# Kernel optimization log

Hardware: AMD Instinct MI355X
Metric: run time of the kernel (lower is better)

The kernel has to match this reference:

```python
import jax, jax.numpy as jnp
import numpy as np

EPS = 1e-7  # keras backend.epsilon()
NUM_ROUTING = 3


def squash(v, axis=-1):
    s2 = jnp.sum(jnp.square(v), axis=axis, keepdims=True)
    scale = s2 / (1.0 + s2) / jnp.sqrt(s2 + EPS)
    return scale * v


def setup_inputs() -> dict:
    key = jax.random.key(0)
    k1, k2 = jax.random.split(key)
    B, I, Q = 64, 2048, 16      # batch, input_num_capsule, input_dim_capsule
    J, P = 32, 32               # num_capsule, dim_capsule
    inputs = jax.random.normal(k1, (B, I, Q), dtype=jnp.float32)
    # glorot-ish scale for W: [num_capsule, input_num_capsule, dim_capsule, input_dim_capsule]
    W = jax.random.normal(k2, (J, I, P, Q), dtype=jnp.float32) * (1.0 / np.sqrt(Q))
    return {"inputs": inputs, "W": W}


def reference(inputs, W):
    # inputs_hat[b,j,i,p] = sum_q inputs[b,i,q] * W[j,i,p,q]
    hat = jnp.einsum('biq,jipq->bjip', inputs, W)
    hat_stop = jax.lax.stop_gradient(hat)
    B, J, I, P = hat.shape
    b = jnp.zeros((B, J, I), dtype=hat.dtype)
    for _ in range(NUM_ROUTING - 1):
        c = jax.nn.softmax(b, axis=1)                       # softmax over num_capsule axis
        v = squash(jnp.einsum('bji,bjip->bjp', c, hat_stop))
        b = b + jnp.einsum('bjp,bjip->bji', v, hat_stop)
    c = jax.nn.softmax(b, axis=1)
    return squash(jnp.einsum('bji,bjip->bjp', c, hat))      # [B, J, P]
```

## Files before the change

### kernel.cpp

```cpp
#include <hip/hip_runtime.h>

typedef _Float16 h8 __attribute__((ext_vector_type(8)));
typedef _Float16 h4 __attribute__((ext_vector_type(4)));
typedef float f4 __attribute__((ext_vector_type(4)));

constexpr int NB = 64;
constexpr int NI = 2048;
constexpr int NQ = 16;
constexpr int NJ = 32;
constexpr int NP = 32;
constexpr int NIP = NI / 2;
constexpr int VSZ = NB * NJ * NP;


__global__ __launch_bounds__(256)
void zero_kernel(f4* __restrict__ p)
{
    const f4 z = {0.f, 0.f, 0.f, 0.f};
    p[(size_t)blockIdx.x * 256 + threadIdx.x] = z;
}

__global__ __launch_bounds__(256)
void xpack_kernel(const float* __restrict__ X, h8* __restrict__ xp)
{
    const int ip = blockIdx.x;
    const int t = threadIdx.x;
    const int bf = t >> 6, l = t & 63;
    const int b = (l & 15) + 16 * bf;
    const int i = 2 * ip + (l >= 32 ? 1 : 0);
    const int q0 = ((l >> 4) & 1) * 8;
    const float* xs = X + ((size_t)b * NI + i) * NQ + q0;
    const float4 u = *reinterpret_cast<const float4*>(xs);
    const float4 v = *reinterpret_cast<const float4*>(xs + 4);
    h8 h;
    h[0] = (_Float16)u.x; h[1] = (_Float16)u.y; h[2] = (_Float16)u.z; h[3] = (_Float16)u.w;
    h[4] = (_Float16)v.x; h[5] = (_Float16)v.y; h[6] = (_Float16)v.z; h[7] = (_Float16)v.w;
    xp[(size_t)(ip * 4 + bf) * 64 + l] = h;
}

__device__ inline float sqscale(float s2)
{
    return s2 / ((1.f + s2) * sqrtf(s2 + 1e-7f));
}

__global__ __launch_bounds__(512)
void wacc_kernel(const float* __restrict__ Wg, const h8* __restrict__ xp,
                 h8* __restrict__ wp, float* __restrict__ ACC)
{
    const int t = threadIdx.x, wv = t >> 6, l = t & 63;
    const int j = blockIdx.x >> 4, is = blockIdx.x & 15;
    const int ioff = (l >= 32) ? 1 : 0;
    const int q0 = ((l >> 4) & 1) * 8;
    const int pbase = is * 64 + wv * 8;

    f4 D[2][4];
#pragma unroll
    for (int pf = 0; pf < 2; ++pf)
#pragma unroll
        for (int bf = 0; bf < 4; ++bf) { f4 Z = {0.f, 0.f, 0.f, 0.f}; D[pf][bf] = Z; }

    const float* wgl = Wg + ((size_t)j * NI + ioff) * (NP * NQ) + (size_t)(l & 15) * NQ + q0;

    f4 u0, u1, v0, v1;
    {
        const float* s0 = wgl + (size_t)(2 * pbase) * (NP * NQ);
        u0 = *reinterpret_cast<const f4*>(s0);
        u1 = *reinterpret_cast<const f4*>(s0 + 4);
        v0 = *reinterpret_cast<const f4*>(s0 + 16 * NQ);
        v1 = *reinterpret_cast<const f4*>(s0 + 16 * NQ + 4);
    }
    h8 B0, B1, B2, B3;
    {
        const h8* xpb = xp + (size_t)pbase * 4 * 64 + l;
        B0 = xpb[0]; B1 = xpb[64]; B2 = xpb[128]; B3 = xpb[192];
    }

#pragma unroll 1
    for (int ipl = 0; ipl < 8; ++ipl) {
        const int ipg = pbase + ipl;
        const int nip = (ipl < 7) ? ipg + 1 : ipg;
        f4 nu0, nu1, nv0, nv1;
        {
            const float* s0 = wgl + (size_t)(2 * nip) * (NP * NQ);
            nu0 = *reinterpret_cast<const f4*>(s0);
            nu1 = *reinterpret_cast<const f4*>(s0 + 4);
            nv0 = *reinterpret_cast<const f4*>(s0 + 16 * NQ);
            nv1 = *reinterpret_cast<const f4*>(s0 + 16 * NQ + 4);
        }
        h8 nB0, nB1, nB2, nB3;
        {
            const h8* xpb = xp + (size_t)nip * 4 * 64 + l;
            nB0 = xpb[0]; nB1 = xpb[64]; nB2 = xpb[128]; nB3 = xpb[192];
        }

        h8 A0, A1;
#pragma unroll
        for (int e = 0; e < 4; ++e) {
            A0[e] = (_Float16)u0[e]; A0[e + 4] = (_Float16)u1[e];
            A1[e] = (_Float16)v0[e]; A1[e + 4] = (_Float16)v1[e];
        }
        const size_t wo = ((size_t)j * NIP + ipg) * 2 * 64 + l;
        wp[wo] = A0;
        wp[wo + 64] = A1;
        D[0][0] = __builtin_amdgcn_mfma_f32_16x16x32_f16(A0, B0, D[0][0], 0, 0, 0);
        D[1][0] = __builtin_amdgcn_mfma_f32_16x16x32_f16(A1, B0, D[1][0], 0, 0, 0);
        D[0][1] = __builtin_amdgcn_mfma_f32_16x16x32_f16(A0, B1, D[0][1], 0, 0, 0);
        D[1][1] = __builtin_amdgcn_mfma_f32_16x16x32_f16(A1, B1, D[1][1], 0, 0, 0);
        D[0][2] = __builtin_amdgcn_mfma_f32_16x16x32_f16(A0, B2, D[0][2], 0, 0, 0);
        D[1][2] = __builtin_amdgcn_mfma_f32_16x16x32_f16(A1, B2, D[1][2], 0, 0, 0);
        D[0][3] = __builtin_amdgcn_mfma_f32_16x16x32_f16(A0, B3, D[0][3], 0, 0, 0);
        D[1][3] = __builtin_amdgcn_mfma_f32_16x16x32_f16(A1, B3, D[1][3], 0, 0, 0);
        u0 = nu0; u1 = nu1; v0 = nv0; v1 = nv1;
        B0 = nB0; B1 = nB1; B2 = nB2; B3 = nB3;
    }

    __shared__ float R[8][64 * 36];
#pragma unroll
    for (int pf = 0; pf < 2; ++pf)
#pragma unroll
        for (int bf = 0; bf < 4; ++bf) {
            const int b = (l & 15) + 16 * bf, p = (l >> 4) * 4 + 16 * pf;
            *reinterpret_cast<f4*>(&R[wv][b * 36 + p]) = D[pf][bf];
        }
    __syncthreads();
#pragma unroll
    for (int k = 0; k < 4; ++k) {
        const int id = t + k * 512;
        const int b = id >> 5, p = id & 31;
        float s = 0.f;
#pragma unroll
        for (int w8 = 0; w8 < 8; ++w8) s += R[w8][b * 36 + p];
        atomicAdd(ACC + ((size_t)b * NJ + j) * NP + p, s);
    }
}

template <int SMODE>
__global__ __launch_bounds__(512)
void logits_kernel(const h8* __restrict__ wp, const h8* __restrict__ xp,
                   const float* __restrict__ U1, const float* __restrict__ U2,
                   _Float16* __restrict__ cp)
{
    __shared__ float L[8][32][64];
    const int t = threadIdx.x, wv = t >> 6, l = t & 63;
    const int i0 = blockIdx.x * 8;
    const int ip0 = blockIdx.x * 4;
    const bool lo = l >= 32;
    h8 zh;
#pragma unroll
    for (int e = 0; e < 8; ++e) zh[e] = (_Float16)0.f;

#pragma unroll 1
    for (int jj = 0; jj < 4; ++jj) {
        const int j = wv * 4 + jj;

        float sreg[4][8];
#pragma unroll
        for (int bf = 0; bf < 4; ++bf) {
            const int b = (l & 15) + 16 * bf;
            const size_t base = ((size_t)b * NJ + j) * NP + (l >> 4) * 4;
            float va[8];
#pragma unroll
            for (int pf = 0; pf < 2; ++pf) {
                const f4 u = *reinterpret_cast<const f4*>(U1 + base + 16 * pf);
#pragma unroll
                for (int r = 0; r < 4; ++r) va[pf * 4 + r] = u[r] * (1.f / 32.f);
            }
            float s2 = 0.f;
#pragma unroll
            for (int e = 0; e < 8; ++e) s2 += va[e] * va[e];
            s2 += __shfl_xor(s2, 16);
            s2 += __shfl_xor(s2, 32);
            const float sc1 = sqscale(s2);
#pragma unroll
            for (int e = 0; e < 8; ++e) sreg[bf][e] = va[e] * sc1;

            if (SMODE == 1) {
                float vb[8];
#pragma unroll
                for (int pf = 0; pf < 2; ++pf) {
                    const f4 u = *reinterpret_cast<const f4*>(U2 + base + 16 * pf);
#pragma unroll
                    for (int r = 0; r < 4; ++r) vb[pf * 4 + r] = u[r];
                }
                float t2 = 0.f;
#pragma unroll
                for (int e = 0; e < 8; ++e) t2 += vb[e] * vb[e];
                t2 += __shfl_xor(t2, 16);
                t2 += __shfl_xor(t2, 32);
                const float sc2 = sqscale(t2);
#pragma unroll
                for (int e = 0; e < 8; ++e) sreg[bf][e] += vb[e] * sc2;
            }
        }

        const h8* wj = wp + (size_t)j * NIP * 2 * 64 + l;
        h8 A0 = wj[(size_t)ip0 * 128];
        h8 A1 = wj[(size_t)ip0 * 128 + 64];

#pragma unroll 1
        for (int ipl = 0; ipl < 4; ++ipl) {
            const int ipg = ip0 + ipl;
            const int nip = (ipl < 3) ? ipg + 1 : ipg;
            h8 nA0 = wj[(size_t)nip * 128];
            h8 nA1 = wj[(size_t)nip * 128 + 64];

            const h8* xpb = xp + (size_t)ipg * 4 * 64 + l;
            h8 B[4];
#pragma unroll
            for (int bf = 0; bf < 4; ++bf) B[bf] = xpb[bf * 64];

#pragma unroll
            for (int half = 0; half < 2; ++half) {
                f4 D[2][4];
#pragma unroll
                for (int pf = 0; pf < 2; ++pf)
#pragma unroll
                    for (int bf = 0; bf < 4; ++bf) { f4 Z = {0.f, 0.f, 0.f, 0.f}; D[pf][bf] = Z; }
#pragma unroll
                for (int bf = 0; bf < 4; ++bf) {
                    const h8 Bm = ((half == 0) == lo) ? zh : B[bf];
                    D[0][bf] = __builtin_amdgcn_mfma_f32_16x16x32_f16(A0, Bm, D[0][bf], 0, 0, 0);
                    D[1][bf] = __builtin_amdgcn_mfma_f32_16x16x32_f16(A1, Bm, D[1][bf], 0, 0, 0);
                }
                float part[4];
#pragma unroll
                for (int bf = 0; bf < 4; ++bf) {
                    float p_ = 0.f;
#pragma unroll
                    for (int pf = 0; pf < 2; ++pf)
#pragma unroll
                        for (int r = 0; r < 4; ++r) p_ += sreg[bf][pf * 4 + r] * D[pf][bf][r];
                    p_ += __shfl_xor(p_, 16);
                    p_ += __shfl_xor(p_, 32);
                    part[bf] = p_;
                }
                const int hb = l >> 4;
                const float wval = hb == 0 ? part[0] : hb == 1 ? part[1] : hb == 2 ? part[2] : part[3];
                L[ipl * 2 + half][j][(l & 15) + 16 * hb] = wval;
            }
            A0 = nA0; A1 = nA1;
        }
    }
    __syncthreads();

    {
        const int b = t & 63, ii = t >> 6;
        float lv[32];
        float m = -1e30f;
#pragma unroll
        for (int j = 0; j < 32; ++j) { lv[j] = L[ii][j][b]; m = fmaxf(m, lv[j]); }
        float s = 0.f;
#pragma unroll
        for (int j = 0; j < 32; ++j) { lv[j] = __expf(lv[j] - m); s += lv[j]; }
        const float inv = 1.f / s;
#pragma unroll
        for (int j = 0; j < 32; ++j) L[ii][j][b] = lv[j] * inv;
    }
    __syncthreads();

    {
        const int jw = t >> 4, r = t & 15;
#pragma unroll 1
        for (int ii = 0; ii < 8; ++ii) {
            h4 c4;
#pragma unroll
            for (int e = 0; e < 4; ++e) c4[e] = (_Float16)L[ii][jw][16 * e + r];
            *reinterpret_cast<h4*>(cp + ((size_t)jw * NI + i0 + ii) * 64 + r * 4) = c4;
        }
    }
}

__global__ __launch_bounds__(512)
void accum_kernel(const h8* __restrict__ wp, const h8* __restrict__ xp,
                  const _Float16* __restrict__ cp, float* __restrict__ ACC)
{
    const int t = threadIdx.x, wv = t >> 6, l = t & 63;
    const int j = blockIdx.x >> 4, is = blockIdx.x & 15;
    const int ioff = (l >= 32) ? 1 : 0;

    f4 D[2][4];
#pragma unroll
    for (int pf = 0; pf < 2; ++pf)
#pragma unroll
        for (int bf = 0; bf < 4; ++bf) { f4 Z = {0.f, 0.f, 0.f, 0.f}; D[pf][bf] = Z; }

    const int pbase = is * 64 + wv * 8;
    const h8* wj = wp + (size_t)j * NIP * 2 * 64 + l;
    const _Float16* cj = cp + ((size_t)j * NI + ioff) * 64 + (l & 15) * 4;

    h8 A0 = wj[(size_t)pbase * 128];
    h8 A1 = wj[(size_t)pbase * 128 + 64];
    h8 B0, B1, B2, B3;
    {
        const h8* xpb = xp + (size_t)pbase * 4 * 64 + l;
        B0 = xpb[0]; B1 = xpb[64]; B2 = xpb[128]; B3 = xpb[192];
    }
    h4 c4 = *reinterpret_cast<const h4*>(cj + (size_t)(2 * pbase) * 64);

#pragma unroll 1
    for (int ipl = 0; ipl < 8; ++ipl) {
        const int ipg = pbase + ipl;
        const int nip = (ipl < 7) ? ipg + 1 : ipg;
        h8 nA0 = wj[(size_t)nip * 128];
        h8 nA1 = wj[(size_t)nip * 128 + 64];
        h8 nB0, nB1, nB2, nB3;
        {
            const h8* xpb = xp + (size_t)nip * 4 * 64 + l;
            nB0 = xpb[0]; nB1 = xpb[64]; nB2 = xpb[128]; nB3 = xpb[192];
        }
        h4 nc4 = *reinterpret_cast<const h4*>(cj + (size_t)(2 * nip) * 64);

        h8 b0 = B0 * c4[0], b1 = B1 * c4[1], b2 = B2 * c4[2], b3 = B3 * c4[3];
        D[0][0] = __builtin_amdgcn_mfma_f32_16x16x32_f16(A0, b0, D[0][0], 0, 0, 0);
        D[1][0] = __builtin_amdgcn_mfma_f32_16x16x32_f16(A1, b0, D[1][0], 0, 0, 0);
        D[0][1] = __builtin_amdgcn_mfma_f32_16x16x32_f16(A0, b1, D[0][1], 0, 0, 0);
        D[1][1] = __builtin_amdgcn_mfma_f32_16x16x32_f16(A1, b1, D[1][1], 0, 0, 0);
        D[0][2] = __builtin_amdgcn_mfma_f32_16x16x32_f16(A0, b2, D[0][2], 0, 0, 0);
        D[1][2] = __builtin_amdgcn_mfma_f32_16x16x32_f16(A1, b2, D[1][2], 0, 0, 0);
        D[0][3] = __builtin_amdgcn_mfma_f32_16x16x32_f16(A0, b3, D[0][3], 0, 0, 0);
        D[1][3] = __builtin_amdgcn_mfma_f32_16x16x32_f16(A1, b3, D[1][3], 0, 0, 0);
        A0 = nA0; A1 = nA1; B0 = nB0; B1 = nB1; B2 = nB2; B3 = nB3; c4 = nc4;
    }

    __shared__ float R[8][64 * 36];
#pragma unroll
    for (int pf = 0; pf < 2; ++pf)
#pragma unroll
        for (int bf = 0; bf < 4; ++bf) {
            const int b = (l & 15) + 16 * bf, p = (l >> 4) * 4 + 16 * pf;
            *reinterpret_cast<f4*>(&R[wv][b * 36 + p]) = D[pf][bf];
        }
    __syncthreads();
#pragma unroll
    for (int k = 0; k < 4; ++k) {
        const int id = t + k * 512;
        const int b = id >> 5, p = id & 31;
        float s = 0.f;
#pragma unroll
        for (int w8 = 0; w8 < 8; ++w8) s += R[w8][b * 36 + p];
        atomicAdd(ACC + ((size_t)b * NJ + j) * NP + p, s);
    }
}

__global__ __launch_bounds__(256)
void squash_kernel(const float* __restrict__ U, float* __restrict__ OUT)
{
    const int t   = threadIdx.x;
    const int row = blockIdx.x * 8 + (t >> 5);
    const int p   = t & 31;
    const float val = U[row * 32 + p];
    float sq = val * val;
#pragma unroll
    for (int d = 1; d < 32; d <<= 1) sq += __shfl_xor(sq, d);
    OUT[row * 32 + p] = val * sqscale(sq);
}

extern "C" void kernel_launch(void* const* d_in, const int* in_sizes, int n_in,
                              void* d_out, int out_size, void* d_ws, size_t ws_size,
                              hipStream_t stream)
{
    const float* X  = (const float*)d_in[0];
    const float* Wg = (const float*)d_in[1];
    float* out = (float*)d_out;

    float* v1u = (float*)d_ws;
    float* v2u = v1u + VSZ;
    float* ou  = v2u + VSZ;
    h8* xp = (h8*)((char*)d_ws + (size_t)3 * VSZ * 4);
    _Float16* cp = (_Float16*)((char*)xp + (size_t)NIP * 4 * 64 * 16);
    h8* wpk = (h8*)((char*)cp + (size_t)NJ * NI * 64 * 2);

    xpack_kernel<<<NIP, 256, 0, stream>>>(X, xp);
    zero_kernel<<<3 * VSZ * 4 / (256 * 16), 256, 0, stream>>>((f4*)d_ws);

    wacc_kernel<<<512, 512, 0, stream>>>(Wg, xp, wpk, v1u);

    logits_kernel<0><<<NI / 8, 512, 0, stream>>>(wpk, xp, v1u, nullptr, cp);
    accum_kernel<<<512, 512, 0, stream>>>(wpk, xp, cp, v2u);

    logits_kernel<1><<<NI / 8, 512, 0, stream>>>(wpk, xp, v1u, v2u, cp);
    accum_kernel<<<512, 512, 0, stream>>>(wpk, xp, cp, ou);

    squash_kernel<<<VSZ / 256, 256, 0, stream>>>(ou, out);
}
```

Before: 139.9 us.

## Fold zeroing into xpack launch and drop software prefetch of x operands

Merges the workspace zeroing kernel into the xpack kernel by adding extra blocks that zero the accumulators, removing one kernel launch. It also removes the register double-buffering of the packed X operands and c coefficients in the wacc, logits and accum loops, loading them just in time instead. This lowers register pressure and may raise occupancy, at the risk of exposing load latency ahead of the MFMAs.

```diff
diff --git a/kernel.cpp b/kernel.cpp
--- a/kernel.cpp
+++ b/kernel.cpp
@@ -11,20 +11,23 @@
 constexpr int NP = 32;
 constexpr int NIP = NI / 2;
 constexpr int VSZ = NB * NJ * NP;
+constexpr int ZBLK = 16;
 
 
 __global__ __launch_bounds__(256)
-void zero_kernel(f4* __restrict__ p)
-{
-    const f4 z = {0.f, 0.f, 0.f, 0.f};
-    p[(size_t)blockIdx.x * 256 + threadIdx.x] = z;
-}
-
-__global__ __launch_bounds__(256)
-void xpack_kernel(const float* __restrict__ X, h8* __restrict__ xp)
-{
-    const int ip = blockIdx.x;
+void xpack_kernel(const float* __restrict__ X, h8* __restrict__ xp,
+                  f4* __restrict__ zbase)
+{
+    const int bid = blockIdx.x;
     const int t = threadIdx.x;
+    if (bid >= NIP) {
+        const f4 z = {0.f, 0.f, 0.f, 0.f};
+        const int base = (bid - NIP) * 256 + t;
+#pragma unroll
+        for (int k = 0; k < 12; ++k) zbase[base + k * 4096] = z;
+        return;
+    }
+    const int ip = bid;
     const int bf = t >> 6, l = t & 63;
     const int b = (l & 15) + 16 * bf;
     const int i = 2 * ip + (l >= 32 ? 1 : 0);
@@ -69,11 +72,6 @@
         v0 = *reinterpret_cast<const f4*>(s0 + 16 * NQ);
         v1 = *reinterpret_cast<const f4*>(s0 + 16 * NQ + 4);
     }
-    h8 B0, B1, B2, B3;
-    {
-        const h8* xpb = xp + (size_t)pbase * 4 * 64 + l;
-        B0 = xpb[0]; B1 = xpb[64]; B2 = xpb[128]; B3 = xpb[192];
-    }
 
 #pragma unroll 1
     for (int ipl = 0; ipl < 8; ++ipl) {
@@ -87,11 +85,8 @@
             nv0 = *reinterpret_cast<const f4*>(s0 + 16 * NQ);
             nv1 = *reinterpret_cast<const f4*>(s0 + 16 * NQ + 4);
         }
-        h8 nB0, nB1, nB2, nB3;
-        {
-            const h8* xpb = xp + (size_t)nip * 4 * 64 + l;
-            nB0 = xpb[0]; nB1 = xpb[64]; nB2 = xpb[128]; nB3 = xpb[192];
-        }
+        const h8* xpb = xp + (size_t)ipg * 4 * 64 + l;
+        const h8 B0 = xpb[0], B1 = xpb[64], B2 = xpb[128], B3 = xpb[192];
 
         h8 A0, A1;
 #pragma unroll
@@ -111,7 +106,6 @@
         D[0][3] = __builtin_amdgcn_mfma_f32_16x16x32_f16(A0, B3, D[0][3], 0, 0, 0);
         D[1][3] = __builtin_amdgcn_mfma_f32_16x16x32_f16(A1, B3, D[1][3], 0, 0, 0);
         u0 = nu0; u1 = nu1; v0 = nv0; v1 = nv1;
-        B0 = nB0; B1 = nB1; B2 = nB2; B3 = nB3;
     }
 
     __shared__ float R[8][64 * 36];
@@ -205,9 +199,6 @@
             h8 nA1 = wj[(size_t)nip * 128 + 64];
 
             const h8* xpb = xp + (size_t)ipg * 4 * 64 + l;
-            h8 B[4];
-#pragma unroll
-            for (int bf = 0; bf < 4; ++bf) B[bf] = xpb[bf * 64];
 
 #pragma unroll
             for (int half = 0; half < 2; ++half) {
@@ -217,10 +208,15 @@
 #pragma unroll
                     for (int bf = 0; bf < 4; ++bf) { f4 Z = {0.f, 0.f, 0.f, 0.f}; D[pf][bf] = Z; }
 #pragma unroll
-                for (int bf = 0; bf < 4; ++bf) {
-                    const h8 Bm = ((half == 0) == lo) ? zh : B[bf];
-                    D[0][bf] = __builtin_amdgcn_mfma_f32_16x16x32_f16(A0, Bm, D[0][bf], 0, 0, 0);
-                    D[1][bf] = __builtin_amdgcn_mfma_f32_16x16x32_f16(A1, Bm, D[1][bf], 0, 0, 0);
+                for (int bfp = 0; bfp < 2; ++bfp) {
+                    const h8 Ba = xpb[(2 * bfp) * 64];
+                    const h8 Bb = xpb[(2 * bfp + 1) * 64];
+                    const h8 Bma = ((half == 0) == lo) ? zh : Ba;
+                    const h8 Bmb = ((half == 0) == lo) ? zh : Bb;
+                    D[0][2 * bfp]     = __builtin_amdgcn_mfma_f32_16x16x32_f16(A0, Bma, D[0][2 * bfp], 0, 0, 0);
+                    D[1][2 * bfp]     = __builtin_amdgcn_mfma_f32_16x16x32_f16(A1, Bma, D[1][2 * bfp], 0, 0, 0);
+                    D[0][2 * bfp + 1] = __builtin_amdgcn_mfma_f32_16x16x32_f16(A0, Bmb, D[0][2 * bfp + 1], 0, 0, 0);
+                    D[1][2 * bfp + 1] = __builtin_amdgcn_mfma_f32_16x16x32_f16(A1, Bmb, D[1][2 * bfp + 1], 0, 0, 0);
                 }
                 float part[4];
 #pragma unroll
@@ -290,12 +286,6 @@
 
     h8 A0 = wj[(size_t)pbase * 128];
     h8 A1 = wj[(size_t)pbase * 128 + 64];
-    h8 B0, B1, B2, B3;
-    {
-        const h8* xpb = xp + (size_t)pbase * 4 * 64 + l;
-        B0 = xpb[0]; B1 = xpb[64]; B2 = xpb[128]; B3 = xpb[192];
-    }
-    h4 c4 = *reinterpret_cast<const h4*>(cj + (size_t)(2 * pbase) * 64);
 
 #pragma unroll 1
     for (int ipl = 0; ipl < 8; ++ipl) {
@@ -303,14 +293,14 @@
         const int nip = (ipl < 7) ? ipg + 1 : ipg;
         h8 nA0 = wj[(size_t)nip * 128];
         h8 nA1 = wj[(size_t)nip * 128 + 64];
-        h8 nB0, nB1, nB2, nB3;
-        {
-            const h8* xpb = xp + (size_t)nip * 4 * 64 + l;
-            nB0 = xpb[0]; nB1 = xpb[64]; nB2 = xpb[128]; nB3 = xpb[192];
-        }
-        h4 nc4 = *reinterpret_cast<const h4*>(cj + (size_t)(2 * nip) * 64);
-
-        h8 b0 = B0 * c4[0], b1 = B1 * c4[1], b2 = B2 * c4[2], b3 = B3 * c4[3];
+
+        const h8* xpb = xp + (size_t)ipg * 4 * 64 + l;
+        const h4 c4 = *reinterpret_cast<const h4*>(cj + (size_t)(2 * ipg) * 64);
+        const h8 b0 = xpb[0] * c4[0];
+        const h8 b1 = xpb[64] * c4[1];
+        const h8 b2 = xpb[128] * c4[2];
+        const h8 b3 = xpb[192] * c4[3];
+
         D[0][0] = __builtin_amdgcn_mfma_f32_16x16x32_f16(A0, b0, D[0][0], 0, 0, 0);
         D[1][0] = __builtin_amdgcn_mfma_f32_16x16x32_f16(A1, b0, D[1][0], 0, 0, 0);
         D[0][1] = __builtin_amdgcn_mfma_f32_16x16x32_f16(A0, b1, D[0][1], 0, 0, 0);
@@ -319,7 +309,7 @@
         D[1][2] = __builtin_amdgcn_mfma_f32_16x16x32_f16(A1, b2, D[1][2], 0, 0, 0);
         D[0][3] = __builtin_amdgcn_mfma_f32_16x16x32_f16(A0, b3, D[0][3], 0, 0, 0);
         D[1][3] = __builtin_amdgcn_mfma_f32_16x16x32_f16(A1, b3, D[1][3], 0, 0, 0);
-        A0 = nA0; A1 = nA1; B0 = nB0; B1 = nB1; B2 = nB2; B3 = nB3; c4 = nc4;
+        A0 = nA0; A1 = nA1;
     }
 
     __shared__ float R[8][64 * 36];
@@ -370,8 +360,7 @@
     _Float16* cp = (_Float16*)((char*)xp + (size_t)NIP * 4 * 64 * 16);
     h8* wpk = (h8*)((char*)cp + (size_t)NJ * NI * 64 * 2);
 
-    xpack_kernel<<<NIP, 256, 0, stream>>>(X, xp);
-    zero_kernel<<<3 * VSZ * 4 / (256 * 16), 256, 0, stream>>>((f4*)d_ws);
+    xpack_kernel<<<NIP + ZBLK, 256, 0, stream>>>(X, xp, (f4*)d_ws);
 
     wacc_kernel<<<512, 512, 0, stream>>>(Wg, xp, wpk, v1u);
 
```

Measured after the change: 143.2 us. 1.02x slower.
